# Optimization experiments

Measured on AMD Instinct MI355X. Metric: run time of the kernel, lower is better.

Reference implementation:

```python
import jax, jax.numpy as jnp
import numpy as np
from jax import lax

D_MODEL = 512
CLASS_NUM = 8000
MAX_LEN = 80
VOCAB = 8002  # len(char2idx): chars + sos/eos
SOS_IDX = 0


def setup_inputs() -> dict:
    key = jax.random.key(0)
    ks = jax.random.split(key, 16)
    T, B, D, V, C = 128, 128, D_MODEL, VOCAB, CLASS_NUM
    s = 1.0 / np.sqrt(D)
    inp = {
        "inputs": jax.random.normal(ks[0], (T, B, D), jnp.float32),
        # additive attention params (query_size=key_size=hidden_size=D)
        "Wq": jax.random.normal(ks[1], (D, D), jnp.float32) * s,
        "bq": jnp.zeros((D,), jnp.float32),
        "Wk": jax.random.normal(ks[2], (D, D), jnp.float32) * s,
        "bk": jnp.zeros((D,), jnp.float32),
        "v": jax.random.normal(ks[3], (D,), jnp.float32) * s,
        # GRUCell: input_size = 2*D, hidden_size = D (PyTorch layout)
        "W_ih": jax.random.normal(ks[4], (3 * D, 2 * D), jnp.float32) * s,
        "b_ih": jnp.zeros((3 * D,), jnp.float32),
        "W_hh": jax.random.normal(ks[5], (3 * D, D), jnp.float32) * s,
        "b_hh": jnp.zeros((3 * D,), jnp.float32),
        # embedding table and classifier
        "emb": jax.random.normal(ks[6], (V, D), jnp.float32),
        "Wc": jax.random.normal(ks[7], (C, D), jnp.float32) * s,
        "bc": jnp.zeros((C,), jnp.float32),
    }
    return inp


def _gru_cell(x, h, W_ih, b_ih, W_hh, b_hh):
    # PyTorch GRUCell math
    gi = x @ W_ih.T + b_ih  # [B, 3D]
    gh = h @ W_hh.T + b_hh  # [B, 3D]
    i_r, i_z, i_n = jnp.split(gi, 3, axis=1)
    h_r, h_z, h_n = jnp.split(gh, 3, axis=1)
    r = jax.nn.sigmoid(i_r + h_r)
    z = jax.nn.sigmoid(i_z + h_z)
    n = jnp.tanh(i_n + r * h_n)
    return (1.0 - z) * n + z * h


def reference(inputs, Wq, bq, Wk, bk, v, W_ih, b_ih, W_hh, b_hh, emb, Wc, bc):
    T, B, D = inputs.shape
    # Attention is called as attention(inputs, keys) with keys = inputs each
    # step -> weights are loop-invariant; compute the context once.
    e = jnp.tanh(inputs @ Wq.T + bq + inputs @ Wk.T + bk) @ v  # [T, B]
    att = jax.nn.softmax(e, axis=0)[..., None]  # [T, B, 1]
    c = jnp.sum(att * inputs, axis=0)  # [B, D]

    h0 = inputs[0]  # initial GRU hidden = first encoder frame
    out0 = emb[jnp.full((B,), SOS_IDX, dtype=jnp.int32)]  # sos embedding

    def step(carry, _):
        h, out = carry
        x = jnp.concatenate([out, c], axis=1)  # [B, 2D]
        h = _gru_cell(x, h, W_ih, b_ih, W_hh, b_hh)
        pred = h @ Wc.T + bc  # [B, class_num]
        top1 = jnp.argmax(pred, axis=1)  # greedy decode (eval mode)
        return (h, emb[top1]), pred

    _, preds = lax.scan(step, (h0, out0), None, length=MAX_LEN)
    return preds  # [max_len, B, class_num]
```

## Files before the change

kernel.cpp:

```cpp
#include <hip/hip_runtime.h>
#include <cstdint>
#include <cstddef>

#define D_MOD 512
#define TH3   1536
#define CLS   8000
#define MAXLEN 80
#define B_SZ  128
#define T_LEN 128
#define NK0   16
#define EGI_ROWS 8000

typedef __attribute__((ext_vector_type(8))) __bf16 bf16x8;
typedef __attribute__((ext_vector_type(8))) unsigned short u16x8;
typedef __attribute__((ext_vector_type(4))) float f32x4;

__device__ __forceinline__ unsigned short f2bf(float x) {
    unsigned u = __float_as_uint(x);
    unsigned r = ((u >> 16) & 1u) + 0x7fffu;
    return (unsigned short)((u + r) >> 16);
}
__device__ __forceinline__ float bf2f(unsigned short h) {
    return __uint_as_float(((unsigned)h) << 16);
}
__device__ __forceinline__ f32x4 mfma16(u16x8 a, u16x8 b, f32x4 c) {
    return __builtin_amdgcn_mfma_f32_16x16x32_bf16(
        __builtin_bit_cast(bf16x8, a), __builtin_bit_cast(bf16x8, b), c, 0, 0, 0);
}
__device__ __forceinline__ void conv8(const float* __restrict__ p, u16x8& hi, u16x8& lo) {
    float4 f0 = *(const float4*)p;
    float4 f1 = *(const float4*)(p + 4);
    float fs[8] = {f0.x, f0.y, f0.z, f0.w, f1.x, f1.y, f1.z, f1.w};
    #pragma unroll
    for (int j = 0; j < 8; ++j) {
        unsigned short h = f2bf(fs[j]);
        hi[j] = h;
        lo[j] = f2bf(fs[j] - bf2f(h));
    }
}
__device__ __forceinline__ unsigned long long packkey(float v, int n) {
    unsigned u = __float_as_uint(v);
    u = (u & 0x80000000u) ? ~u : (u | 0x80000000u);
    return ((unsigned long long)u << 32) | (unsigned)(~(unsigned)n);
}
__device__ __forceinline__ unsigned long long shfl_xor_u64(unsigned long long x, int mask) {
    unsigned lo = (unsigned)x, hi = (unsigned)(x >> 32);
    lo = __shfl_xor(lo, mask, 16);
    hi = __shfl_xor(hi, mask, 16);
    return ((unsigned long long)hi << 32) | lo;
}
__device__ __forceinline__ size_t pk_off(int n, int k) {
    int tile = n >> 4, lr = n & 15, k0i = k >> 5, lk = (k >> 3) & 3, e = k & 7;
    return ((size_t)(tile * NK0 + k0i) * 64 + (lk * 16 + lr)) * 8 + e;
}

__global__ __launch_bounds__(256) void cvt2p_kernel(
    const float* __restrict__ s1, const float* __restrict__ s2, int ld,
    long total4, unsigned short* __restrict__ hi, unsigned short* __restrict__ lo)
{
    long i4 = (long)blockIdx.x * 256 + threadIdx.x;
    if (i4 >= total4) return;
    long r = i4 >> 7;
    int c = (int)(i4 & 127) * 4;
    float4 a = *(const float4*)(s1 + r * (long)ld + c);
    if (s2) {
        float4 b = *(const float4*)(s2 + r * (long)ld + c);
        a.x += b.x; a.y += b.y; a.z += b.z; a.w += b.w;
    }
    float xs[4] = {a.x, a.y, a.z, a.w};
    unsigned short hs[4], ls[4];
    #pragma unroll
    for (int j = 0; j < 4; ++j) {
        hs[j] = f2bf(xs[j]);
        ls[j] = f2bf(xs[j] - bf2f(hs[j]));
    }
    size_t o = pk_off((int)r, c);
    *(ushort4*)(hi + o) = make_ushort4(hs[0], hs[1], hs[2], hs[3]);
    *(ushort4*)(lo + o) = make_ushort4(ls[0], ls[1], ls[2], ls[3]);
}

template<bool GATHER_CONV, bool CONVB, bool ADD2D, bool ARGMAX, int NS, int KS>
__device__ __forceinline__ void gemm_ks2(
    const unsigned short* __restrict__ Ahi, const unsigned short* __restrict__ Alo,
    const float* __restrict__ Afp, const unsigned long long* __restrict__ gslot,
    const unsigned short* __restrict__ Bhi, const unsigned short* __restrict__ Blo,
    const float* __restrict__ Bfp,
    const float* __restrict__ bias, const float* __restrict__ D2,
    float* __restrict__ C, int ldc,
    unsigned long long* __restrict__ aslot, int bx, int by)
{
    static_assert(NS * KS == 8, "8 waves per block");
    __shared__ float red[(KS - 1) * NS * 576];
    const int tid = threadIdx.x;
    const int w = tid >> 6, lane = tid & 63;
    const int lr = lane & 15, lk = lane >> 4;
    const int ns = w % NS, ks = w / NS;
    const int m0 = by * 16;
    const int n0 = (bx * NS + ns) * 32;
    const int tA = by;
    const int tB0 = n0 >> 4, tB1 = tB0 + 1;

    const float* paf = nullptr;
    if constexpr (GATHER_CONV) {
        int g = gslot ? (int)(~(unsigned)gslot[m0 + lr]) : (m0 + lr);
        paf = Afp + (size_t)g * D_MOD + lk * 8;
    }
    const float *pb0f = nullptr, *pb1f = nullptr;
    if constexpr (CONVB) {
        pb0f = Bfp + (size_t)(n0 + lr) * D_MOD + lk * 8;
        pb1f = Bfp + (size_t)(n0 + 16 + lr) * D_MOD + lk * 8;
    }

    f32x4 acc0 = (f32x4){0.f, 0.f, 0.f, 0.f};
    f32x4 acc1 = (f32x4){0.f, 0.f, 0.f, 0.f};

    const int kBeg = ks * (NK0 / KS), kEnd = kBeg + (NK0 / KS);
    for (int k0i = kBeg; k0i < kEnd; ++k0i) {
        u16x8 ah, al, b0h, b0l, b1h, b1l;
        if constexpr (GATHER_CONV) {
            conv8(paf + k0i * 32, ah, al);
        } else {
            size_t oA = ((size_t)(tA * NK0 + k0i) * 64 + lane) * 8;
            ah = *(const u16x8*)(Ahi + oA); al = *(const u16x8*)(Alo + oA);
        }
        if constexpr (CONVB) {
            conv8(pb0f + k0i * 32, b0h, b0l);
            conv8(pb1f + k0i * 32, b1h, b1l);
        } else {
            size_t oB0 = ((size_t)(tB0 * NK0 + k0i) * 64 + lane) * 8;
            size_t oB1 = ((size_t)(tB1 * NK0 + k0i) * 64 + lane) * 8;
            b0h = *(const u16x8*)(Bhi + oB0); b0l = *(const u16x8*)(Blo + oB0);
            b1h = *(const u16x8*)(Bhi + oB1); b1l = *(const u16x8*)(Blo + oB1);
        }
        acc0 = mfma16(ah, b0h, acc0);
        acc0 = mfma16(ah, b0l, acc0);
        acc0 = mfma16(al, b0h, acc0);
        acc1 = mfma16(ah, b1h, acc1);
        acc1 = mfma16(ah, b1l, acc1);
        acc1 = mfma16(al, b1h, acc1);
    }

    float af[8];
    #pragma unroll
    for (int i = 0; i < 4; ++i) { af[i] = acc0[i]; af[4 + i] = acc1[i]; }

    if (ks > 0) {
        const int slot = (ks - 1) * NS + ns;
        #pragma unroll
        for (int i = 0; i < 8; ++i) red[slot * 576 + lane * 9 + i] = af[i];
    }
    __syncthreads();
    if (ks == 0) {
        #pragma unroll
        for (int j = 1; j < KS; ++j) {
            const int slot = (j - 1) * NS + ns;
            #pragma unroll
            for (int i = 0; i < 8; ++i) af[i] += red[slot * 576 + lane * 9 + i];
        }
        #pragma unroll
        for (int r = 0; r < 4; ++r) {
            const int row = m0 + lk * 4 + r;
            unsigned long long kmax = 0ull;
            #pragma unroll
            for (int ni = 0; ni < 2; ++ni) {
                const int col = n0 + ni * 16 + lr;
                float val = af[ni * 4 + r];
                if (bias) val += bias[col];
                if constexpr (ADD2D) val += D2[(size_t)row * ldc + col];
                C[(size_t)row * ldc + col] = val;
                if constexpr (ARGMAX) {
                    unsigned long long k = packkey(val, col);
                    if (k > kmax) kmax = k;
                }
            }
            if constexpr (ARGMAX) {
                #pragma unroll
                for (int off = 1; off < 16; off <<= 1) {
                    unsigned long long o = shfl_xor_u64(kmax, off);
                    if (o > kmax) kmax = o;
                }
                if (lr == 0) atomicMax(&aslot[row], kmax);
            }
        }
    }
}

template<int G>
__device__ __forceinline__ bool xcd_map(int p, int& bx, int& by) {
    int x = p & 7, s = p >> 3;
    by = s & 7;
    bx = x * G + (s >> 3);
    return true;
}

__global__ __launch_bounds__(512) void egi_kernel(
    const float* __restrict__ emb,
    const unsigned short* __restrict__ WihaHi, const unsigned short* __restrict__ WihaLo,
    float* __restrict__ Egi)
{
    int p = blockIdx.x;
    int x = p & 7, s = p >> 3;
    int by = s % 500, bx = x * 6 + s / 500;
    gemm_ks2<true, false, false, false, 1, 8>(nullptr, nullptr, emb, nullptr,
        WihaHi, WihaLo, nullptr, nullptr, nullptr, Egi, TH3, nullptr, bx, by);
}

__global__ __launch_bounds__(512) void gh_kernel(
    const unsigned short* __restrict__ hHi, const unsigned short* __restrict__ hLo,
    const unsigned short* __restrict__ WhhHi, const unsigned short* __restrict__ WhhLo,
    const float* __restrict__ b_hh, float* __restrict__ gh)
{
    int bx, by;
    xcd_map<6>(blockIdx.x, bx, by);
    gemm_ks2<false, false, false, false, 1, 8>(hHi, hLo, nullptr, nullptr,
        WhhHi, WhhLo, nullptr, b_hh, nullptr, gh, TH3, nullptr, bx, by);
}

__global__ __launch_bounds__(512) void step_dual_kernel(
    const unsigned short* __restrict__ hHi, const unsigned short* __restrict__ hLo,
    const unsigned short* __restrict__ WhhHi, const unsigned short* __restrict__ WhhLo,
    const float* __restrict__ b_hh,
    const float* __restrict__ emb, const unsigned long long* __restrict__ sPrev,
    const unsigned short* __restrict__ WihaHi, const unsigned short* __restrict__ WihaLo,
    const float* __restrict__ gc,
    float* __restrict__ gh, float* __restrict__ gi)
{
    int p = blockIdx.x;
    const int z = (p >= 384);
    p -= z * 384;
    int bx, by;
    xcd_map<6>(p, bx, by);
    if (z == 0)
        gemm_ks2<false, false, false, false, 1, 8>(hHi, hLo, nullptr, nullptr,
            WhhHi, WhhLo, nullptr, b_hh, nullptr, gh, TH3, nullptr, bx, by);
    else
        gemm_ks2<true, false, true, false, 1, 8>(nullptr, nullptr, emb, sPrev,
            WihaHi, WihaLo, nullptr, nullptr, gc, gi, TH3, nullptr, bx, by);
}

__global__ __launch_bounds__(512) void gemm128_kernel(
    const unsigned short* __restrict__ Ahi, const unsigned short* __restrict__ Alo,
    const unsigned short* __restrict__ Bhi, const unsigned short* __restrict__ Blo,
    const float* __restrict__ bias, float* __restrict__ C)
{
    int bx, by;
    xcd_map<6>(blockIdx.x, bx, by);
    gemm_ks2<false, false, false, false, 1, 8>(Ahi, Alo, nullptr, nullptr,
        Bhi, Blo, nullptr, bias, nullptr, C, TH3, nullptr, bx, by);
}

template<bool CONVB>
__global__ __launch_bounds__(512) void cls_kernel(
    const unsigned short* __restrict__ hHi, const unsigned short* __restrict__ hLo,
    const unsigned short* __restrict__ WcHi, const unsigned short* __restrict__ WcLo,
    const float* __restrict__ Wc, const float* __restrict__ bc,
    float* __restrict__ C, unsigned long long* __restrict__ aslot)
{
    int bx, by;
    xcd_map<16>(blockIdx.x, bx, by);
    if (bx >= 125) return;
    gemm_ks2<false, CONVB, false, true, 2, 4>(hHi, hLo, nullptr, nullptr,
        WcHi, WcLo, Wc, bc, nullptr, C, CLS, aslot, bx, by);
}

__global__ __launch_bounds__(256) void attn_e_mfma(
    const float* __restrict__ inp,
    const unsigned short* __restrict__ WqkHi, const unsigned short* __restrict__ WqkLo,
    const float* __restrict__ bq, const float* __restrict__ bk,
    const float* __restrict__ v, float* __restrict__ e)
{
    __shared__ __align__(16) unsigned short Ah[32][40];
    __shared__ __align__(16) unsigned short Al[32][40];
    __shared__ float red[4][32];
    const int tid = threadIdx.x, w = tid >> 6, lane = tid & 63;
    const int lr = lane & 15, lk = lane >> 4;
    const int m0 = blockIdx.x * 32;
    const int srow = tid >> 3, scol = (tid & 7) * 4;

    f32x4 acc[2][8];
    #pragma unroll
    for (int i = 0; i < 2; ++i)
        #pragma unroll
        for (int j = 0; j < 8; ++j) acc[i][j] = (f32x4){0.f, 0.f, 0.f, 0.f};

    for (int k0i = 0; k0i < NK0; ++k0i) {
        float4 x = *(const float4*)(inp + (size_t)(m0 + srow) * D_MOD + k0i * 32 + scol);
        float xs[4] = {x.x, x.y, x.z, x.w};
        #pragma unroll
        for (int j = 0; j < 4; ++j) {
            unsigned short h = f2bf(xs[j]);
            Ah[srow][scol + j] = h;
            Al[srow][scol + j] = f2bf(xs[j] - bf2f(h));
        }
        __syncthreads();
        u16x8 a[2][2];
        #pragma unroll
        for (int mi = 0; mi < 2; ++mi) {
            a[mi][0] = *(const u16x8*)&Ah[mi * 16 + lr][lk * 8];
            a[mi][1] = *(const u16x8*)&Al[mi * 16 + lr][lk * 8];
        }
        #pragma unroll
        for (int nf = 0; nf < 8; ++nf) {
            const int tile = w * 8 + nf;
            size_t ob = ((size_t)(tile * NK0 + k0i) * 64 + lane) * 8;
            u16x8 bh = *(const u16x8*)(WqkHi + ob);
            u16x8 bl = *(const u16x8*)(WqkLo + ob);
            #pragma unroll
            for (int mi = 0; mi < 2; ++mi) {
                acc[mi][nf] = mfma16(a[mi][0], bh, acc[mi][nf]);
                acc[mi][nf] = mfma16(a[mi][0], bl, acc[mi][nf]);
                acc[mi][nf] = mfma16(a[mi][1], bh, acc[mi][nf]);
            }
        }
        __syncthreads();
    }

    float ep[2][4];
    #pragma unroll
    for (int mi = 0; mi < 2; ++mi)
        #pragma unroll
        for (int r = 0; r < 4; ++r) ep[mi][r] = 0.f;
    #pragma unroll
    for (int nf = 0; nf < 8; ++nf) {
        const int col = w * 128 + nf * 16 + lr;
        const float bb = bq[col] + bk[col];
        const float vv = v[col];
        #pragma unroll
        for (int mi = 0; mi < 2; ++mi)
            #pragma unroll
            for (int r = 0; r < 4; ++r)
                ep[mi][r] += vv * tanhf(acc[mi][nf][r] + bb);
    }
    #pragma unroll
    for (int mi = 0; mi < 2; ++mi)
        #pragma unroll
        for (int r = 0; r < 4; ++r) {
            float s = ep[mi][r];
            #pragma unroll
            for (int off = 1; off < 16; off <<= 1) s += __shfl_xor(s, off, 16);
            if (lr == 0) red[w][mi * 16 + lk * 4 + r] = s;
        }
    __syncthreads();
    if (tid < 32) e[m0 + tid] = red[0][tid] + red[1][tid] + red[2][tid] + red[3][tid];
}

__global__ __launch_bounds__(256) void softmax_ctx_kernel(
    const float* __restrict__ inp, const float* __restrict__ e,
    unsigned short* __restrict__ cHi, unsigned short* __restrict__ cLo,
    float* __restrict__ h1, unsigned short* __restrict__ h1Hi, unsigned short* __restrict__ h1Lo,
    unsigned long long* __restrict__ slots)
{
    __shared__ float att[T_LEN];
    __shared__ float red;
    const int b = blockIdx.x, tid = threadIdx.x;
    float val = -1e30f;
    if (tid < T_LEN) { val = e[(size_t)tid * B_SZ + b]; att[tid] = val; }
    __syncthreads();
    if (tid < 64) {
        float m = fmaxf(att[tid], att[tid + 64]);
        #pragma unroll
        for (int off = 32; off; off >>= 1) m = fmaxf(m, __shfl_xor(m, off));
        if (tid == 0) red = m;
    }
    __syncthreads();
    const float mx = red;
    __syncthreads();
    if (tid < T_LEN) att[tid] = expf(val - mx);
    __syncthreads();
    if (tid < 64) {
        float s = att[tid] + att[tid + 64];
        #pragma unroll
        for (int off = 32; off; off >>= 1) s += __shfl_xor(s, off);
        if (tid == 0) red = s;
    }
    __syncthreads();
    const float inv = 1.f / red;

    const int d0 = tid * 2;
    float ax = 0.f, ay = 0.f;
    for (int t = 0; t < T_LEN; ++t) {
        float a = att[t];
        float2 x = *(const float2*)(inp + ((size_t)t * B_SZ + b) * D_MOD + d0);
        ax += a * x.x; ay += a * x.y;
        if (t == 0) {
            *(float2*)(h1 + (size_t)b * D_MOD + d0) = x;
            unsigned short hx = f2bf(x.x), hy = f2bf(x.y);
            h1Hi[pk_off(b, d0)]     = hx;
            h1Hi[pk_off(b, d0 + 1)] = hy;
            h1Lo[pk_off(b, d0)]     = f2bf(x.x - bf2f(hx));
            h1Lo[pk_off(b, d0 + 1)] = f2bf(x.y - bf2f(hy));
        }
    }
    ax *= inv; ay *= inv;
    unsigned short cx = f2bf(ax), cy = f2bf(ay);
    cHi[pk_off(b, d0)]     = cx;
    cHi[pk_off(b, d0 + 1)] = cy;
    cLo[pk_off(b, d0)]     = f2bf(ax - bf2f(cx));
    cLo[pk_off(b, d0 + 1)] = f2bf(ay - bf2f(cy));
    if (tid == 0) {
        slots[b] = 0ull;
        slots[B_SZ + b] = 0x00000000FFFFFFFFull;
    }
}

__global__ __launch_bounds__(512) void gru_combine(
    const float* __restrict__ gh, const float* __restrict__ gi,
    const float* __restrict__ hPrev, float* __restrict__ hCur,
    unsigned short* __restrict__ hHiC, unsigned short* __restrict__ hLoC,
    unsigned long long* __restrict__ slotCur)
{
    const int b = blockIdx.x, k = threadIdx.x;
    const float* gib = gi + (size_t)b * TH3;
    const float* ghb = gh + (size_t)b * TH3;
    float r = 1.f / (1.f + expf(-(gib[k] + ghb[k])));
    float z = 1.f / (1.f + expf(-(gib[k + 512] + ghb[k + 512])));
    float n = tanhf(gib[k + 1024] + r * ghb[k + 1024]);
    float h = hPrev[(size_t)b * D_MOD + k];
    float hv = (1.f - z) * n + z * h;
    hCur[(size_t)b * D_MOD + k] = hv;
    unsigned short hh = f2bf(hv);
    size_t o = pk_off(b, k);
    hHiC[o] = hh;
    hLoC[o] = f2bf(hv - bf2f(hh));
    if (k == 0) slotCur[b] = 0ull;
}

__global__ __launch_bounds__(512) void gru_combine_egi(
    const float* __restrict__ gh, const float* __restrict__ Egi,
    const float* __restrict__ gc, const unsigned long long* __restrict__ sPrev,
    const float* __restrict__ hPrev, float* __restrict__ hCur,
    unsigned short* __restrict__ hHiC, unsigned short* __restrict__ hLoC,
    unsigned long long* __restrict__ slotCur)
{
    const int b = blockIdx.x, k = threadIdx.x;
    const int sel = (int)(~(unsigned)sPrev[b]);
    const float* gib = Egi + (size_t)sel * TH3;
    const float* gcb = gc + (size_t)b * TH3;
    const float* ghb = gh + (size_t)b * TH3;
    float gi0 = gib[k] + gcb[k];
    float gi1 = gib[k + 512] + gcb[k + 512];
    float gi2 = gib[k + 1024] + gcb[k + 1024];
    float r = 1.f / (1.f + expf(-(gi0 + ghb[k])));
    float z = 1.f / (1.f + expf(-(gi1 + ghb[k + 512])));
    float n = tanhf(gi2 + r * ghb[k + 1024]);
    float h = hPrev[(size_t)b * D_MOD + k];
    float hv = (1.f - z) * n + z * h;
    hCur[(size_t)b * D_MOD + k] = hv;
    unsigned short hh = f2bf(hv);
    size_t o = pk_off(b, k);
    hHiC[o] = hh;
    hLoC[o] = f2bf(hv - bf2f(hh));
    if (k == 0) slotCur[b] = 0ull;
}

extern "C" void kernel_launch(void* const* d_in, const int* in_sizes, int n_in,
                              void* d_out, int out_size, void* d_ws, size_t ws_size,
                              hipStream_t stream)
{
    const float* inp  = (const float*)d_in[0];
    const float* Wq   = (const float*)d_in[1];
    const float* bq   = (const float*)d_in[2];
    const float* Wk   = (const float*)d_in[3];
    const float* bk   = (const float*)d_in[4];
    const float* v    = (const float*)d_in[5];
    const float* W_ih = (const float*)d_in[6];
    const float* b_ih = (const float*)d_in[7];
    const float* W_hh = (const float*)d_in[8];
    const float* b_hh = (const float*)d_in[9];
    const float* emb  = (const float*)d_in[10];
    const float* Wc   = (const float*)d_in[11];
    const float* bc   = (const float*)d_in[12];
    float* out = (float*)d_out;

    char* base = (char*)d_ws;
    size_t off = 0;
    auto alloc = [&](size_t bytes) -> char* {
        char* q = base + off;
        off += (bytes + 255) & ~(size_t)255;
        return q;
    };
    typedef unsigned short us;
    us* WqkHi  = (us*)alloc(512 * 512 * 2);
    us* WqkLo  = (us*)alloc(512 * 512 * 2);
    us* WhhHi  = (us*)alloc((size_t)TH3 * 512 * 2);
    us* WhhLo  = (us*)alloc((size_t)TH3 * 512 * 2);
    us* WihaHi = (us*)alloc((size_t)TH3 * 512 * 2);
    us* WihaLo = (us*)alloc((size_t)TH3 * 512 * 2);
    us* WihbHi = (us*)alloc((size_t)TH3 * 512 * 2);
    us* WihbLo = (us*)alloc((size_t)TH3 * 512 * 2);
    float* e   = (float*)alloc(T_LEN * B_SZ * 4);
    us* cHi    = (us*)alloc(B_SZ * 512 * 2);
    us* cLo    = (us*)alloc(B_SZ * 512 * 2);
    float* gc  = (float*)alloc((size_t)B_SZ * TH3 * 4);
    float* gh  = (float*)alloc((size_t)B_SZ * TH3 * 4);
    float* gi  = (float*)alloc((size_t)B_SZ * TH3 * 4);
    float* hF[2]; us* hHi[2]; us* hLo[2];
    hF[0] = (float*)alloc(B_SZ * 512 * 4);
    hF[1] = (float*)alloc(B_SZ * 512 * 4);
    hHi[0] = (us*)alloc(B_SZ * 512 * 2);
    hHi[1] = (us*)alloc(B_SZ * 512 * 2);
    hLo[0] = (us*)alloc(B_SZ * 512 * 2);
    hLo[1] = (us*)alloc(B_SZ * 512 * 2);
    unsigned long long* slots = (unsigned long long*)alloc(2 * B_SZ * 8);
    us* WcHi = (us*)alloc((size_t)CLS * 512 * 2);
    us* WcLo = (us*)alloc((size_t)CLS * 512 * 2);
    const bool PREB = (off <= ws_size);
    float* Egi = (float*)alloc((size_t)EGI_ROWS * TH3 * 4);
    const bool EGIB = (off <= ws_size);

    cvt2p_kernel<<<(512 * 128) / 256, 256, 0, stream>>>(Wq, Wk, 512, 512L * 128, WqkHi, WqkLo);
    cvt2p_kernel<<<(TH3 * 128) / 256, 256, 0, stream>>>(W_hh, nullptr, 512, (long)TH3 * 128, WhhHi, WhhLo);
    cvt2p_kernel<<<(TH3 * 128) / 256, 256, 0, stream>>>(W_ih, nullptr, 1024, (long)TH3 * 128, WihaHi, WihaLo);
    cvt2p_kernel<<<(TH3 * 128) / 256, 256, 0, stream>>>(W_ih + 512, nullptr, 1024, (long)TH3 * 128, WihbHi, WihbLo);
    if (PREB)
        cvt2p_kernel<<<(CLS * 128) / 256, 256, 0, stream>>>(Wc, nullptr, 512, (long)CLS * 128, WcHi, WcLo);
    if (EGIB)
        egi_kernel<<<8 * 6 * 500, 512, 0, stream>>>(emb, WihaHi, WihaLo, Egi);

    attn_e_mfma<<<(T_LEN * B_SZ) / 32, 256, 0, stream>>>(inp, WqkHi, WqkLo, bq, bk, v, e);
    softmax_ctx_kernel<<<B_SZ, 256, 0, stream>>>(inp, e, cHi, cLo, hF[1], hHi[1], hLo[1], slots);
    gemm128_kernel<<<384, 512, 0, stream>>>(cHi, cLo, WihbHi, WihbLo, b_ih, gc);

    for (int t = 0; t < MAXLEN; ++t) {
        const int pi = (t + 1) & 1, ci = t & 1;
        unsigned long long* sPrev = slots + pi * B_SZ;
        unsigned long long* sCur  = slots + ci * B_SZ;

        if (EGIB) {
            gh_kernel<<<384, 512, 0, stream>>>(
                hHi[pi], hLo[pi], WhhHi, WhhLo, b_hh, gh);
            gru_combine_egi<<<B_SZ, 512, 0, stream>>>(
                gh, Egi, gc, sPrev, hF[pi], hF[ci], hHi[ci], hLo[ci], sCur);
        } else {
            step_dual_kernel<<<768, 512, 0, stream>>>(
                hHi[pi], hLo[pi], WhhHi, WhhLo, b_hh,
                emb, sPrev, WihaHi, WihaLo, gc, gh, gi);
            gru_combine<<<B_SZ, 512, 0, stream>>>(
                gh, gi, hF[pi], hF[ci], hHi[ci], hLo[ci], sCur);
        }
        if (PREB)
            cls_kernel<false><<<1024, 512, 0, stream>>>(
                hHi[ci], hLo[ci], WcHi, WcLo, nullptr, bc,
                out + (size_t)t * B_SZ * CLS, sCur);
        else
            cls_kernel<true><<<1024, 512, 0, stream>>>(
                hHi[ci], hLo[ci], nullptr, nullptr, Wc, bc,
                out + (size_t)t * B_SZ * CLS, sCur);
    }
}
```

Baseline: 2.945 ms.

## Fuse next-step W_hh GEMM into classifier kernel launch

In the precomputed-Egi path, the hidden-state gate GEMM for step t+1 now runs in the same launch as the classifier GEMM for step t, since both read the same new hidden state. The first gh is computed before the loop. This removes one kernel launch per step and lets the small gh GEMM fill idle CUs alongside the classifier blocks. The shared reduction buffer is moved from the device function into each kernel so both branches share one allocation, sized for the larger 7*576 case. That larger allocation may lower occupancy for the classifier blocks.

```diff
diff --git a/kernel.cpp b/kernel.cpp
--- a/kernel.cpp
+++ b/kernel.cpp
@@ -81,6 +81,7 @@
 
 template<bool GATHER_CONV, bool CONVB, bool ADD2D, bool ARGMAX, int NS, int KS>
 __device__ __forceinline__ void gemm_ks2(
+    float* __restrict__ red,
     const unsigned short* __restrict__ Ahi, const unsigned short* __restrict__ Alo,
     const float* __restrict__ Afp, const unsigned long long* __restrict__ gslot,
     const unsigned short* __restrict__ Bhi, const unsigned short* __restrict__ Blo,
@@ -90,7 +91,6 @@
     unsigned long long* __restrict__ aslot, int bx, int by)
 {
     static_assert(NS * KS == 8, "8 waves per block");
-    __shared__ float red[(KS - 1) * NS * 576];
     const int tid = threadIdx.x;
     const int w = tid >> 6, lane = tid & 63;
     const int lr = lane & 15, lk = lane >> 4;
@@ -198,10 +198,11 @@
     const unsigned short* __restrict__ WihaHi, const unsigned short* __restrict__ WihaLo,
     float* __restrict__ Egi)
 {
+    __shared__ float red[7 * 576];
     int p = blockIdx.x;
     int x = p & 7, s = p >> 3;
     int by = s % 500, bx = x * 6 + s / 500;
-    gemm_ks2<true, false, false, false, 1, 8>(nullptr, nullptr, emb, nullptr,
+    gemm_ks2<true, false, false, false, 1, 8>(red, nullptr, nullptr, emb, nullptr,
         WihaHi, WihaLo, nullptr, nullptr, nullptr, Egi, TH3, nullptr, bx, by);
 }
 
@@ -210,10 +211,36 @@
     const unsigned short* __restrict__ WhhHi, const unsigned short* __restrict__ WhhLo,
     const float* __restrict__ b_hh, float* __restrict__ gh)
 {
+    __shared__ float red[7 * 576];
     int bx, by;
     xcd_map<6>(blockIdx.x, bx, by);
-    gemm_ks2<false, false, false, false, 1, 8>(hHi, hLo, nullptr, nullptr,
+    gemm_ks2<false, false, false, false, 1, 8>(red, hHi, hLo, nullptr, nullptr,
         WhhHi, WhhLo, nullptr, b_hh, nullptr, gh, TH3, nullptr, bx, by);
+}
+
+template<bool CONVB>
+__global__ __launch_bounds__(512) void cls_gh_kernel(
+    const unsigned short* __restrict__ hHi, const unsigned short* __restrict__ hLo,
+    const unsigned short* __restrict__ WcHi, const unsigned short* __restrict__ WcLo,
+    const float* __restrict__ Wc, const float* __restrict__ bc,
+    float* __restrict__ C, unsigned long long* __restrict__ aslot,
+    const unsigned short* __restrict__ WhhHi, const unsigned short* __restrict__ WhhLo,
+    const float* __restrict__ b_hh, float* __restrict__ gh)
+{
+    __shared__ float red[7 * 576];
+    const int p = blockIdx.x;
+    if (p < 1024) {
+        int bx, by;
+        xcd_map<16>(p, bx, by);
+        if (bx >= 125) return;
+        gemm_ks2<false, CONVB, false, true, 2, 4>(red, hHi, hLo, nullptr, nullptr,
+            WcHi, WcLo, Wc, bc, nullptr, C, CLS, aslot, bx, by);
+    } else {
+        int bx, by;
+        xcd_map<6>(p - 1024, bx, by);
+        gemm_ks2<false, false, false, false, 1, 8>(red, hHi, hLo, nullptr, nullptr,
+            WhhHi, WhhLo, nullptr, b_hh, nullptr, gh, TH3, nullptr, bx, by);
+    }
 }
 
 __global__ __launch_bounds__(512) void step_dual_kernel(
@@ -225,16 +252,17 @@
     const float* __restrict__ gc,
     float* __restrict__ gh, float* __restrict__ gi)
 {
+    __shared__ float red[7 * 576];
     int p = blockIdx.x;
     const int z = (p >= 384);
     p -= z * 384;
     int bx, by;
     xcd_map<6>(p, bx, by);
     if (z == 0)
-        gemm_ks2<false, false, false, false, 1, 8>(hHi, hLo, nullptr, nullptr,
+        gemm_ks2<false, false, false, false, 1, 8>(red, hHi, hLo, nullptr, nullptr,
             WhhHi, WhhLo, nullptr, b_hh, nullptr, gh, TH3, nullptr, bx, by);
     else
-        gemm_ks2<true, false, true, false, 1, 8>(nullptr, nullptr, emb, sPrev,
+        gemm_ks2<true, false, true, false, 1, 8>(red, nullptr, nullptr, emb, sPrev,
             WihaHi, WihaLo, nullptr, nullptr, gc, gi, TH3, nullptr, bx, by);
 }
 
@@ -243,9 +271,10 @@
     const unsigned short* __restrict__ Bhi, const unsigned short* __restrict__ Blo,
     const float* __restrict__ bias, float* __restrict__ C)
 {
+    __shared__ float red[7 * 576];
     int bx, by;
     xcd_map<6>(blockIdx.x, bx, by);
-    gemm_ks2<false, false, false, false, 1, 8>(Ahi, Alo, nullptr, nullptr,
+    gemm_ks2<false, false, false, false, 1, 8>(red, Ahi, Alo, nullptr, nullptr,
         Bhi, Blo, nullptr, bias, nullptr, C, TH3, nullptr, bx, by);
 }
 
@@ -256,10 +285,11 @@
     const float* __restrict__ Wc, const float* __restrict__ bc,
     float* __restrict__ C, unsigned long long* __restrict__ aslot)
 {
+    __shared__ float red[3 * 2 * 576];
     int bx, by;
     xcd_map<16>(blockIdx.x, bx, by);
     if (bx >= 125) return;
-    gemm_ks2<false, CONVB, false, true, 2, 4>(hHi, hLo, nullptr, nullptr,
+    gemm_ks2<false, CONVB, false, true, 2, 4>(red, hHi, hLo, nullptr, nullptr,
         WcHi, WcLo, Wc, bc, nullptr, C, CLS, aslot, bx, by);
 }
 
@@ -521,30 +551,45 @@
     softmax_ctx_kernel<<<B_SZ, 256, 0, stream>>>(inp, e, cHi, cLo, hF[1], hHi[1], hLo[1], slots);
     gemm128_kernel<<<384, 512, 0, stream>>>(cHi, cLo, WihbHi, WihbLo, b_ih, gc);
 
-    for (int t = 0; t < MAXLEN; ++t) {
-        const int pi = (t + 1) & 1, ci = t & 1;
-        unsigned long long* sPrev = slots + pi * B_SZ;
-        unsigned long long* sCur  = slots + ci * B_SZ;
-
-        if (EGIB) {
-            gh_kernel<<<384, 512, 0, stream>>>(
-                hHi[pi], hLo[pi], WhhHi, WhhLo, b_hh, gh);
+    if (EGIB) {
+        gh_kernel<<<384, 512, 0, stream>>>(hHi[1], hLo[1], WhhHi, WhhLo, b_hh, gh);
+        for (int t = 0; t < MAXLEN; ++t) {
+            const int pi = (t + 1) & 1, ci = t & 1;
+            unsigned long long* sPrev = slots + pi * B_SZ;
+            unsigned long long* sCur  = slots + ci * B_SZ;
+
             gru_combine_egi<<<B_SZ, 512, 0, stream>>>(
                 gh, Egi, gc, sPrev, hF[pi], hF[ci], hHi[ci], hLo[ci], sCur);
-        } else {
+            if (PREB)
+                cls_gh_kernel<false><<<1408, 512, 0, stream>>>(
+                    hHi[ci], hLo[ci], WcHi, WcLo, nullptr, bc,
+                    out + (size_t)t * B_SZ * CLS, sCur,
+                    WhhHi, WhhLo, b_hh, gh);
+            else
+                cls_gh_kernel<true><<<1408, 512, 0, stream>>>(
+                    hHi[ci], hLo[ci], nullptr, nullptr, Wc, bc,
+                    out + (size_t)t * B_SZ * CLS, sCur,
+                    WhhHi, WhhLo, b_hh, gh);
+        }
+    } else {
+        for (int t = 0; t < MAXLEN; ++t) {
+            const int pi = (t + 1) & 1, ci = t & 1;
+            unsigned long long* sPrev = slots + pi * B_SZ;
+            unsigned long long* sCur  = slots + ci * B_SZ;
+
             step_dual_kernel<<<768, 512, 0, stream>>>(
                 hHi[pi], hLo[pi], WhhHi, WhhLo, b_hh,
                 emb, sPrev, WihaHi, WihaLo, gc, gh, gi);
             gru_combine<<<B_SZ, 512, 0, stream>>>(
                 gh, gi, hF[pi], hF[ci], hHi[ci], hLo[ci], sCur);
-        }
-        if (PREB)
-            cls_kernel<false><<<1024, 512, 0, stream>>>(
-                hHi[ci], hLo[ci], WcHi, WcLo, nullptr, bc,
-                out + (size_t)t * B_SZ * CLS, sCur);
-        else
-            cls_kernel<true><<<1024, 512, 0, stream>>>(
-                hHi[ci], hLo[ci], nullptr, nullptr, Wc, bc,
-                out + (size_t)t * B_SZ * CLS, sCur);
-    }
-}
+            if (PREB)
+                cls_kernel<false><<<1024, 512, 0, stream>>>(
+                    hHi[ci], hLo[ci], WcHi, WcLo, nullptr, bc,
+                    out + (size_t)t * B_SZ * CLS, sCur);
+            else
+                cls_kernel<true><<<1024, 512, 0, stream>>>(
+                    hHi[ci], hLo[ci], nullptr, nullptr, Wc, bc,
+                    out + (size_t)t * B_SZ * CLS, sCur);
+        }
+    }
+}
```

After: 2.615 ms, median of 2. -11.2%, faster.
